# Performance work log

Measured on AMD Instinct MI355X. Metric: run time of the kernel, lower is better.

The kernel has to match this reference:

```python
import jax, jax.numpy as jnp
import numpy as np

B, T, E, V = 128, 24, 512, 30000
H2 = 2 * 512  # LSTMCell hidden size = 2*hidden_size per original code
IN = 2 * E    # token embedding concat image feature


def setup_inputs() -> dict:
    key = jax.random.key(0)
    ks = jax.random.split(key, 9)
    s = lambda fan: 1.0 / np.sqrt(fan)
    return {
        "features": jax.random.normal(ks[0], (B, E), jnp.float32),
        "captions": jax.random.randint(ks[1], (B, T), 0, V),
        "pad_idx": 0,
        "emb": jax.random.normal(ks[2], (V, E), jnp.float32),
        "W_ih": jax.random.uniform(ks[3], (4 * H2, IN), jnp.float32, -s(H2), s(H2)),
        "W_hh": jax.random.uniform(ks[4], (4 * H2, H2), jnp.float32, -s(H2), s(H2)),
        "b_ih": jax.random.uniform(ks[5], (4 * H2,), jnp.float32, -s(H2), s(H2)),
        "b_hh": jax.random.uniform(ks[6], (4 * H2,), jnp.float32, -s(H2), s(H2)),
        "W_out": jax.random.uniform(ks[7], (V, H2), jnp.float32, -s(H2), s(H2)),
        "b_out": jax.random.uniform(ks[8], (V,), jnp.float32, -s(H2), s(H2)),
    }


def reference(features, captions, pad_idx, emb, W_ih, W_hh, b_ih, b_hh, W_out, b_out):
    b = captions.shape[0]
    tok = emb[captions]                                   # [B,T,E]
    pad = jnp.broadcast_to(emb[pad_idx][None, None, :], (b, 1, E))
    seq = jnp.concatenate([pad, tok], axis=1)             # [B,T+1,E]
    feat = jnp.broadcast_to(features[:, None, :], (b, seq.shape[1], features.shape[1]))
    x = jnp.concatenate([seq, feat], axis=2)              # [B,T+1,2E]

    # precompute input-side gate projections for all timesteps (batched GEMM)
    xg = jnp.einsum('bti,gi->btg', x, W_ih) + b_ih + b_hh  # [B,T+1,4*H2]

    def step(carry, xg_t):
        h, c = carry
        g = xg_t + h @ W_hh.T                             # [B,4*H2]
        i, f, gg, o = jnp.split(g, 4, axis=-1)            # torch gate order i,f,g,o
        i, f, o = jax.nn.sigmoid(i), jax.nn.sigmoid(f), jax.nn.sigmoid(o)
        c = f * c + i * jnp.tanh(gg)
        h = o * jnp.tanh(c)
        return (h, c), h

    h0 = jnp.zeros((b, H2), x.dtype)
    c0 = jnp.zeros((b, H2), x.dtype)
    _, hs = jax.lax.scan(step, (h0, c0), jnp.swapaxes(xg, 0, 1))  # [T+1,B,H2]
    hs = jnp.swapaxes(hs, 0, 1)                           # [B,T+1,H2]

    logits = jnp.einsum('bth,vh->btv', hs, W_out) + b_out  # [B,T+1,V]
    predicted = jnp.transpose(logits[:, :-1, :], (0, 2, 1))  # [B,V,T]
    return predicted
```

## Files before the change

### kernel.cpp

```cpp
#include <hip/hip_runtime.h>
#include <hip/hip_bf16.h>
#include <math.h>

typedef unsigned short ushort_t;
typedef unsigned long long u64;
typedef __bf16 bf16x8 __attribute__((ext_vector_type(8)));
typedef float f32x4 __attribute__((ext_vector_type(4)));

#define BB 128
#define TT 24
#define EE 512
#define VV 30000
#define HH 1024
#define GG 4096
#define MM (BB*TT)

static __device__ __forceinline__ ushort_t f2bf(float x) {
  __hip_bfloat16 h = __float2bfloat16(x);
  return __builtin_bit_cast(ushort_t, h);
}

static __device__ __forceinline__ void gld_lds16(const void* g, void* l) {
  __builtin_amdgcn_global_load_lds((const __attribute__((address_space(1))) void*)g,
                                   (__attribute__((address_space(3))) void*)l, 16, 0, 0);
}


__global__ void cast_bf16_k(const float* __restrict__ s, ushort_t* __restrict__ d, int n4) {
  int i = blockIdx.x * blockDim.x + threadIdx.x;
  int stride = gridDim.x * blockDim.x;
  for (; i < n4; i += stride) {
    float4 v = reinterpret_cast<const float4*>(s)[i];
    ushort4 o;
    o.x = f2bf(v.x); o.y = f2bf(v.y); o.z = f2bf(v.z); o.w = f2bf(v.w);
    reinterpret_cast<ushort4*>(d)[i] = o;
  }
}

__global__ void bias_sum_k(const float* __restrict__ bi, const float* __restrict__ bh,
                           float* __restrict__ bs) {
  int i = blockIdx.x * blockDim.x + threadIdx.x;
  if (i < GG) bs[i] = bi[i] + bh[i];
}

__global__ void build_xa_k(const float* __restrict__ emb, const int* __restrict__ captions,
                           const int* __restrict__ pad_idx, const float* __restrict__ features,
                           ushort_t* __restrict__ xa) {
  int row = blockIdx.x;
  int t = row >> 7;
  int b = row & 127;
  int cap = (t == 0) ? pad_idx[0] : captions[b * TT + (t - 1)];
  const float* s0 = emb + (size_t)cap * EE;
  const float* s1 = features + (size_t)b * EE;
  ushort_t* d = xa + (size_t)row * (2 * EE);
  for (int e = threadIdx.x; e < EE; e += 256) {
    d[e] = f2bf(s0[e]);
    d[EE + e] = f2bf(s1[e]);
  }
}

__global__ void zero_bar_k(int* __restrict__ bar) {
  for (int i = threadIdx.x; i < 768; i += 256)
    __hip_atomic_store(&bar[i], 0, __ATOMIC_RELAXED, __HIP_MEMORY_SCOPE_AGENT);
}

template<int MODE>
__global__ __launch_bounds__(256) void gemm_bt(
    const ushort_t* __restrict__ A,
    const ushort_t* __restrict__ Bm,
    const float* __restrict__ bias,
    float* __restrict__ out,
    int M, int N, int swn, int xn_cnt)
{
  constexpr int K = 1024;
  __shared__ __align__(16) ushort_t As[2][8192];
  __shared__ __align__(16) ushort_t Bs[2][8192];
  const int bid = blockIdx.x;
  const int xcd = bid & 7, c = bid >> 3;
  const int xn = xcd % xn_cnt, xm = xcd / xn_cnt;
  const int nblk = xn * swn + (c % swn);
  const int mblk = xm * (0) + 0;
  (void)mblk;
  const int mb = xm;
  const int n0 = nblk * 128;
  const int m0 = (mb * ((gridDim.x >> 3) / swn) + (c / swn)) * 128;
  const int tid = threadIdx.x, wid = tid >> 6, lane = tid & 63;
  const int wm = (wid >> 1) * 64, wn_ = (wid & 1) * 64;
  const int srow = lane >> 3;
  const int scolsw = ((lane & 7) ^ srow) * 8;
  const int rr = lane & 15, l4 = lane >> 4;
  const int swz = (rr & 7) << 4;
  const int col0 = (((l4 << 4) ^ swz) >> 1);
  const int col1 = (((64 | (l4 << 4)) ^ swz) >> 1);

  f32x4 acc[4][4] = {};

  auto stage = [&](int buf, int k0) {
    #pragma unroll
    for (int p = 0; p < 4; ++p) {
      int ch = p * 4 + wid;
      int row = ch * 8 + srow;
      gld_lds16(A + (size_t)(m0 + row) * K + k0 + scolsw, &As[buf][ch * 512]);
      gld_lds16(Bm + (size_t)(n0 + row) * K + k0 + scolsw, &Bs[buf][ch * 512]);
    }
  };

  stage(0, 0);
  int cur = 0;
  for (int tau = 0; tau < 16; ++tau) {
    if (tau < 15) {
      stage(cur ^ 1, (tau + 1) * 64);
      asm volatile("s_waitcnt vmcnt(8)" ::: "memory");
    } else {
      asm volatile("s_waitcnt vmcnt(0)" ::: "memory");
    }
    __builtin_amdgcn_s_barrier();
    const ushort_t* Ac = As[cur];
    const ushort_t* Bc = Bs[cur];
    #pragma unroll
    for (int kk = 0; kk < 2; ++kk) {
      const int ce = kk ? col1 : col0;
      bf16x8 af[4], bfv[4];
      #pragma unroll
      for (int i = 0; i < 4; ++i)
        af[i] = *reinterpret_cast<const bf16x8*>(Ac + (wm + i * 16 + rr) * 64 + ce);
      #pragma unroll
      for (int j = 0; j < 4; ++j)
        bfv[j] = *reinterpret_cast<const bf16x8*>(Bc + (wn_ + j * 16 + rr) * 64 + ce);
      #pragma unroll
      for (int i = 0; i < 4; ++i)
        #pragma unroll
        for (int j = 0; j < 4; ++j)
          acc[i][j] = __builtin_amdgcn_mfma_f32_16x16x32_bf16(af[i], bfv[j], acc[i][j], 0, 0, 0);
    }
    asm volatile("" ::: "memory");
    __builtin_amdgcn_s_barrier();
    cur ^= 1;
  }

  const int l16 = lane & 15;
  if (MODE == 0) {
    const int t_blk = m0 >> 7;
    #pragma unroll
    for (int i = 0; i < 4; ++i) {
      #pragma unroll
      for (int j = 0; j < 4; ++j) {
        int n = n0 + wn_ + j * 16 + l16;
        float bv = bias[n];
        #pragma unroll
        for (int r = 0; r < 4; ++r) {
          int b = wm + i * 16 + l4 * 4 + r;
          out[((size_t)t_blk * GG + n) * BB + b] = acc[i][j][r] + bv;
        }
      }
    }
  } else {
    #pragma unroll
    for (int i = 0; i < 4; ++i) {
      #pragma unroll
      for (int r = 0; r < 4; ++r) {
        int v = m0 + wm + i * 16 + l4 * 4 + r;
        if (v < M) {
          float bv = bias[v];
          #pragma unroll
          for (int j = 0; j < 4; ++j) {
            int n = n0 + wn_ + j * 16 + l16;
            int bb = n / TT, tq = n - bb * TT;
            out[(size_t)bb * ((size_t)VV * TT) + (size_t)v * TT + tq] = acc[i][j][r] + bv;
          }
        }
      }
    }
  }
}

__global__ __launch_bounds__(512, 1) void lstm_seq_k(
    const ushort_t* __restrict__ Whh,
    const float* __restrict__ xgT,
    ushort_t* __restrict__ hs,
    int* __restrict__ bar)
{
  __shared__ f32x4 red[6][64][4];
  const int tid = threadIdx.x, wid = tid >> 6, lane = tid & 63;
  const int l16 = lane & 15, l4 = lane >> 4;
  const int bid = blockIdx.x;
  const int jblk = bid & 63, mblk = bid >> 6;
  const int j0 = jblk * 16, m0 = mblk * 32;
  const int ks = wid >> 1;
  const int msub = (wid & 1) * 16;
  int* flags = bar;
  int* rel = bar + 256;

  bf16x8 Breg[4][8];
  #pragma unroll
  for (int g = 0; g < 4; ++g) {
    const ushort_t* bp = Whh + ((size_t)(g * 1024 + j0 + l16) << 10) + ks * 256 + l4 * 8;
    #pragma unroll
    for (int kc = 0; kc < 8; ++kc)
      Breg[g][kc] = *reinterpret_cast<const bf16x8*>(bp + kc * 32);
  }
  const int arow = m0 + msub + l16;
  float c_reg[4] = {0.f, 0.f, 0.f, 0.f};

  for (int t = 0; t < TT; ++t) {
    f32x4 acc[4] = {};
    f32x4 xv[4];
    if (ks == 0) {
      const float* xp = xgT + ((size_t)(t * GG + j0 + l16)) * BB + m0 + msub + l4 * 4;
      #pragma unroll
      for (int g = 0; g < 4; ++g)
        xv[g] = *reinterpret_cast<const f32x4*>(xp + (size_t)g * 1024 * BB);
    }
    if (t > 0) {
      const u64* Ab = reinterpret_cast<const u64*>(
          hs + (((size_t)arow * TT + (t - 1)) << 10) + ks * 256 + l4 * 8);
      bf16x8 afs[8];
      #pragma unroll
      for (int kc = 0; kc < 8; ++kc) {
        union { u64 q[2]; bf16x8 v; } u;
        u.q[0] = __hip_atomic_load(Ab + kc * 8,     __ATOMIC_RELAXED, __HIP_MEMORY_SCOPE_AGENT);
        u.q[1] = __hip_atomic_load(Ab + kc * 8 + 1, __ATOMIC_RELAXED, __HIP_MEMORY_SCOPE_AGENT);
        afs[kc] = u.v;
      }
      #pragma unroll
      for (int kc = 0; kc < 8; ++kc)
        #pragma unroll
        for (int g = 0; g < 4; ++g)
          acc[g] = __builtin_amdgcn_mfma_f32_16x16x32_bf16(afs[kc], Breg[g][kc], acc[g], 0, 0, 0);
    }
    if (ks != 0) {
      int slot = (ks - 1) * 2 + (wid & 1);
      #pragma unroll
      for (int g = 0; g < 4; ++g) red[slot][lane][g] = acc[g];
    }
    __syncthreads();
    if (ks == 0) {
      #pragma unroll
      for (int s = 0; s < 3; ++s)
        #pragma unroll
        for (int g = 0; g < 4; ++g)
          acc[g] += red[s * 2 + (wid & 1)][lane][g];
      #pragma unroll
      for (int r = 0; r < 4; ++r) {
        int b = m0 + msub + l4 * 4 + r;
        float gi = acc[0][r] + xv[0][r];
        float gf = acc[1][r] + xv[1][r];
        float gg = acc[2][r] + xv[2][r];
        float go = acc[3][r] + xv[3][r];
        gi = 1.f / (1.f + expf(-gi));
        gf = 1.f / (1.f + expf(-gf));
        go = 1.f / (1.f + expf(-go));
        float cn = gf * c_reg[r] + gi * tanhf(gg);
        c_reg[r] = cn;
        float hn = go * tanhf(cn);
        unsigned hv = (unsigned)f2bf(hn);
        unsigned pv = (unsigned)__shfl_xor((int)hv, 1);
        if (!(l16 & 1)) {
          unsigned pk = (hv & 0xffffu) | (pv << 16);
          __hip_atomic_store(
              reinterpret_cast<unsigned*>(hs + (((size_t)b * TT + t) << 10) + j0 + l16),
              pk, __ATOMIC_RELAXED, __HIP_MEMORY_SCOPE_AGENT);
        }
      }
    }
    if (t < TT - 1) {
      __syncthreads();
      if (bid == 0) {
        if (wid == 0) {
          if (lane == 0)
            __hip_atomic_store(&flags[0], t + 1, __ATOMIC_RELAXED, __HIP_MEMORY_SCOPE_AGENT);
          for (;;) {
            int a0 = __hip_atomic_load(&flags[lane],       __ATOMIC_RELAXED, __HIP_MEMORY_SCOPE_AGENT);
            int a1 = __hip_atomic_load(&flags[lane +  64], __ATOMIC_RELAXED, __HIP_MEMORY_SCOPE_AGENT);
            int a2 = __hip_atomic_load(&flags[lane + 128], __ATOMIC_RELAXED, __HIP_MEMORY_SCOPE_AGENT);
            int a3 = __hip_atomic_load(&flags[lane + 192], __ATOMIC_RELAXED, __HIP_MEMORY_SCOPE_AGENT);
            int mn = min(min(a0, a1), min(a2, a3));
            if (__all(mn >= t + 1)) break;
            __builtin_amdgcn_s_sleep(2);
          }
          if (lane < 8)
            __hip_atomic_store(&rel[lane * 64], t + 1, __ATOMIC_RELAXED, __HIP_MEMORY_SCOPE_AGENT);
        }
      } else {
        if (tid == 0) {
          __hip_atomic_store(&flags[bid], t + 1, __ATOMIC_RELAXED, __HIP_MEMORY_SCOPE_AGENT);
          while (__hip_atomic_load(&rel[(bid & 7) * 64], __ATOMIC_RELAXED, __HIP_MEMORY_SCOPE_AGENT) < t + 1)
            __builtin_amdgcn_s_sleep(4);
        }
      }
      __syncthreads();
    }
  }
}


extern "C" void kernel_launch(void* const* d_in, const int* in_sizes, int n_in,
                              void* d_out, int out_size, void* d_ws, size_t ws_size,
                              hipStream_t stream) {
  const float* features = (const float*)d_in[0];
  const int*   captions = (const int*)d_in[1];
  const int*   pad_idx  = (const int*)d_in[2];
  const float* emb      = (const float*)d_in[3];
  const float* W_ih     = (const float*)d_in[4];
  const float* W_hh     = (const float*)d_in[5];
  const float* b_ih     = (const float*)d_in[6];
  const float* b_hh     = (const float*)d_in[7];
  const float* W_out    = (const float*)d_in[8];
  const float* b_out    = (const float*)d_in[9];
  float* out = (float*)d_out;

  char* w = (char*)d_ws;
  auto carve = [&](size_t bytes) {
    char* p = w;
    w += (bytes + 255) & ~(size_t)255;
    return p;
  };
  ushort_t* Wih_b  = (ushort_t*)carve((size_t)GG * HH * 2);
  ushort_t* Whh_b  = (ushort_t*)carve((size_t)GG * HH * 2);
  ushort_t* Wout_b = (ushort_t*)carve((size_t)30208 * HH * 2);
  ushort_t* xa     = (ushort_t*)carve((size_t)MM * HH * 2);
  float*    xgT    = (float*)carve((size_t)MM * GG * 4);
  ushort_t* hs     = (ushort_t*)carve((size_t)MM * HH * 2);
  float*    bsum   = (float*)carve((size_t)GG * 4);
  int*      bar    = (int*)carve(4096);

  cast_bf16_k<<<dim3(1024), 256, 0, stream>>>(W_ih, Wih_b, GG * HH / 4);
  cast_bf16_k<<<dim3(1024), 256, 0, stream>>>(W_hh, Whh_b, GG * HH / 4);
  cast_bf16_k<<<dim3(2048), 256, 0, stream>>>(W_out, Wout_b, VV * HH / 4);
  bias_sum_k<<<dim3(16), 256, 0, stream>>>(b_ih, b_hh, bsum);
  build_xa_k<<<dim3(MM), 256, 0, stream>>>(emb, captions, pad_idx, features, xa);
  zero_bar_k<<<dim3(1), 256, 0, stream>>>(bar);

  gemm_bt<0><<<dim3(768), 256, 0, stream>>>(xa, Wih_b, bsum, xgT, MM, GG, 8, 4);

  lstm_seq_k<<<dim3(256), 512, 0, stream>>>(Whh_b, xgT, hs, bar);

  gemm_bt<1><<<dim3(5664), 256, 0, stream>>>(Wout_b, hs, b_out, out, VV, MM, 12, 2);
}
```

Measured before the change: 618.5 us.

## Use 256x256-tile 512-thread GEMM with quarter-staged pipeline for logits

Replaces the 128x128 templated GEMM for the output projection with a dedicated kernel that uses 256x256 tiles, 8 waves and 128 KB of double-buffered LDS. Loads are staged in quarters interleaved with MFMA work, and the kernel adds setprio hints and an XCD-aware block mapping. The goal is to cut global/L2 traffic per FLOP and hide load latency in the dominant vocab GEMM. The cost is higher register and LDS pressure, which allows only one block per CU, and the hand-placed waitcnt counts risk ordering errors.

New measurement: 594.6 us. 3.9% less time.

```diff
diff --git a/kernel.cpp b/kernel.cpp
--- a/kernel.cpp
+++ b/kernel.cpp
@@ -14,6 +14,7 @@
 #define HH 1024
 #define GG 4096
 #define MM (BB*TT)
+#define MPAD 30208
 
 static __device__ __forceinline__ ushort_t f2bf(float x) {
   __hip_bfloat16 h = __float2bfloat16(x);
@@ -64,8 +65,7 @@
     __hip_atomic_store(&bar[i], 0, __ATOMIC_RELAXED, __HIP_MEMORY_SCOPE_AGENT);
 }
 
-template<int MODE>
-__global__ __launch_bounds__(256) void gemm_bt(
+__global__ __launch_bounds__(256) void gemm_xg(
     const ushort_t* __restrict__ A,
     const ushort_t* __restrict__ Bm,
     const float* __restrict__ bias,
@@ -79,11 +79,8 @@
   const int xcd = bid & 7, c = bid >> 3;
   const int xn = xcd % xn_cnt, xm = xcd / xn_cnt;
   const int nblk = xn * swn + (c % swn);
-  const int mblk = xm * (0) + 0;
-  (void)mblk;
-  const int mb = xm;
   const int n0 = nblk * 128;
-  const int m0 = (mb * ((gridDim.x >> 3) / swn) + (c / swn)) * 128;
+  const int m0 = (xm * ((gridDim.x >> 3) / swn) + (c / swn)) * 128;
   const int tid = threadIdx.x, wid = tid >> 6, lane = tid & 63;
   const int wm = (wid >> 1) * 64, wn_ = (wid & 1) * 64;
   const int srow = lane >> 3;
@@ -139,35 +136,127 @@
   }
 
   const int l16 = lane & 15;
-  if (MODE == 0) {
-    const int t_blk = m0 >> 7;
-    #pragma unroll
-    for (int i = 0; i < 4; ++i) {
-      #pragma unroll
-      for (int j = 0; j < 4; ++j) {
-        int n = n0 + wn_ + j * 16 + l16;
-        float bv = bias[n];
-        #pragma unroll
-        for (int r = 0; r < 4; ++r) {
-          int b = wm + i * 16 + l4 * 4 + r;
-          out[((size_t)t_blk * GG + n) * BB + b] = acc[i][j][r] + bv;
-        }
-      }
-    }
-  } else {
-    #pragma unroll
-    for (int i = 0; i < 4; ++i) {
+  const int t_blk = m0 >> 7;
+  #pragma unroll
+  for (int i = 0; i < 4; ++i) {
+    #pragma unroll
+    for (int j = 0; j < 4; ++j) {
+      int n = n0 + wn_ + j * 16 + l16;
+      float bv = bias[n];
       #pragma unroll
       for (int r = 0; r < 4; ++r) {
-        int v = m0 + wm + i * 16 + l4 * 4 + r;
-        if (v < M) {
-          float bv = bias[v];
-          #pragma unroll
-          for (int j = 0; j < 4; ++j) {
-            int n = n0 + wn_ + j * 16 + l16;
-            int bb = n / TT, tq = n - bb * TT;
-            out[(size_t)bb * ((size_t)VV * TT) + (size_t)v * TT + tq] = acc[i][j][r] + bv;
-          }
+        int b = wm + i * 16 + l4 * 4 + r;
+        out[((size_t)t_blk * GG + n) * BB + b] = acc[i][j][r] + bv;
+      }
+    }
+  }
+}
+
+__global__ __launch_bounds__(512) void gemm256_logits(
+    const ushort_t* __restrict__ A,
+    const ushort_t* __restrict__ Bm,
+    const float* __restrict__ bias,
+    float* __restrict__ out)
+{
+  constexpr int K = 1024, NT = 16;
+  __shared__ __align__(16) ushort_t As[2][16384];
+  __shared__ __align__(16) ushort_t Bs[2][16384];
+  const int bid = blockIdx.x;
+  const int g = (bid & 7) * 177 + (bid >> 3);
+  const int m0 = (g / 12) * 256, n0 = (g % 12) * 256;
+  const int tid = threadIdx.x, wid = tid >> 6, lane = tid & 63;
+  const int wm2 = wid >> 2, wn4 = wid & 3;
+  const int rr = lane & 15, l4 = lane >> 4;
+  const int col80 = (l4 ^ (rr & 7)) * 8;
+  const int col81 = ((l4 + 4) ^ (rr & 7)) * 8;
+  const int la0 = rr + wm2 * 64;
+  const int lb0 = wn4 * 32 + rr;
+
+  f32x4 acc[8][4] = {};
+
+  auto stage = [&](int buf, int kt, int ct) {
+    const int k0 = kt * 64;
+    #pragma unroll
+    for (int l = 0; l < 2; ++l) {
+      int f = l * 512 + tid;
+      int lr = f >> 3;
+      int ecol = k0 + (((f & 7) ^ (lr & 7)) * 8);
+      if (ct == 0 || ct == 3) {
+        int cc = (ct == 3);
+        int grow = (lr & 63) + ((lr >> 6) << 7) + cc * 64;
+        gld_lds16(A + (size_t)(m0 + grow) * K + ecol,
+                  &As[buf][cc * 8192 + (l * 512 + wid * 64) * 8]);
+      } else {
+        int cc = ct - 1;
+        int grow = ((lr >> 5) << 6) + cc * 32 + (lr & 31);
+        gld_lds16(Bm + (size_t)(n0 + grow) * K + ecol,
+                  &Bs[buf][cc * 8192 + (l * 512 + wid * 64) * 8]);
+      }
+    }
+  };
+
+  #pragma unroll
+  for (int p = 0; p < 4; ++p) stage(0, 0, p);
+  asm volatile("s_waitcnt vmcnt(4)" ::: "memory");
+  __builtin_amdgcn_s_barrier();
+
+  int cur = 0;
+  for (int g2 = 0; g2 < NT; ++g2) {
+    const int buf = cur, bufn = cur ^ 1;
+    const int ktn = (g2 + 1 < NT) ? g2 + 1 : g2;
+    bf16x8 aF[4][2], bF[2][2];
+    #pragma unroll
+    for (int p = 0; p < 4; ++p) {
+      stage(bufn, ktn, p);
+      if ((p & 1) == 0) {
+        #pragma unroll
+        for (int mi = 0; mi < 4; ++mi) {
+          const ushort_t* ab = &As[buf][(p >> 1) * 8192 + (la0 + mi * 16) * 64];
+          aF[mi][0] = *reinterpret_cast<const bf16x8*>(ab + col80);
+          aF[mi][1] = *reinterpret_cast<const bf16x8*>(ab + col81);
+        }
+      }
+      #pragma unroll
+      for (int ni = 0; ni < 2; ++ni) {
+        const int nf = (p & 1) * 2 + ni;
+        const ushort_t* bb2 = &Bs[buf][(nf >> 1) * 8192 + (lb0 + (nf & 1) * 16) * 64];
+        bF[ni][0] = *reinterpret_cast<const bf16x8*>(bb2 + col80);
+        bF[ni][1] = *reinterpret_cast<const bf16x8*>(bb2 + col81);
+      }
+      asm volatile("s_waitcnt lgkmcnt(0)" ::: "memory");
+      __builtin_amdgcn_sched_barrier(0);
+      __builtin_amdgcn_s_setprio(1);
+      #pragma unroll
+      for (int mi = 0; mi < 4; ++mi)
+        #pragma unroll
+        for (int ni = 0; ni < 2; ++ni) {
+          f32x4 a = acc[(p >> 1) * 4 + mi][(p & 1) * 2 + ni];
+          a = __builtin_amdgcn_mfma_f32_16x16x32_bf16(aF[mi][0], bF[ni][0], a, 0, 0, 0);
+          a = __builtin_amdgcn_mfma_f32_16x16x32_bf16(aF[mi][1], bF[ni][1], a, 0, 0, 0);
+          acc[(p >> 1) * 4 + mi][(p & 1) * 2 + ni] = a;
+        }
+      __builtin_amdgcn_s_setprio(0);
+      if (p != 2) asm volatile("s_waitcnt vmcnt(4)" ::: "memory");
+      __builtin_amdgcn_s_barrier();
+    }
+    cur ^= 1;
+  }
+  asm volatile("s_waitcnt vmcnt(0)" ::: "memory");
+
+  const int vbase = m0 + wm2 * 128;
+  const int nbase = n0 + wn4 * 64;
+  #pragma unroll
+  for (int mf = 0; mf < 8; ++mf) {
+    #pragma unroll
+    for (int r = 0; r < 4; ++r) {
+      int v = vbase + mf * 16 + l4 * 4 + r;
+      if (v < VV) {
+        float bv = bias[v];
+        #pragma unroll
+        for (int nf = 0; nf < 4; ++nf) {
+          int n = nbase + nf * 16 + rr;
+          int bb = n / TT, tq = n - bb * TT;
+          out[(size_t)bb * ((size_t)VV * TT) + (size_t)v * TT + tq] = acc[mf][nf][r] + bv;
         }
       }
     }
@@ -317,7 +406,7 @@
   };
   ushort_t* Wih_b  = (ushort_t*)carve((size_t)GG * HH * 2);
   ushort_t* Whh_b  = (ushort_t*)carve((size_t)GG * HH * 2);
-  ushort_t* Wout_b = (ushort_t*)carve((size_t)30208 * HH * 2);
+  ushort_t* Wout_b = (ushort_t*)carve((size_t)MPAD * HH * 2);
   ushort_t* xa     = (ushort_t*)carve((size_t)MM * HH * 2);
   float*    xgT    = (float*)carve((size_t)MM * GG * 4);
   ushort_t* hs     = (ushort_t*)carve((size_t)MM * HH * 2);
@@ -331,9 +420,9 @@
   build_xa_k<<<dim3(MM), 256, 0, stream>>>(emb, captions, pad_idx, features, xa);
   zero_bar_k<<<dim3(1), 256, 0, stream>>>(bar);
 
-  gemm_bt<0><<<dim3(768), 256, 0, stream>>>(xa, Wih_b, bsum, xgT, MM, GG, 8, 4);
+  gemm_xg<<<dim3(768), 256, 0, stream>>>(xa, Wih_b, bsum, xgT, MM, GG, 8, 4);
 
   lstm_seq_k<<<dim3(256), 512, 0, stream>>>(Whh_b, xgT, hs, bar);
 
-  gemm_bt<1><<<dim3(5664), 256, 0, stream>>>(Wout_b, hs, b_out, out, VV, MM, 12, 2);
-}
+  gemm256_logits<<<dim3(1416), 512, 0, stream>>>(Wout_b, hs, b_out, out);
+}
```
